# Performance work log

Hardware: AMD Instinct MI355X
Metric: run time of the kernel (lower is better)

The kernel has to match this reference:

```python
import jax, jax.numpy as jnp
import numpy as np

HEAD_NUMS = 8
LN_EPS = 1e-5


def _layernorm(x, g, b):
    m = jnp.mean(x, axis=-1, keepdims=True)
    v = jnp.var(x, axis=-1, keepdims=True)
    return (x - m) * jax.lax.rsqrt(v + LN_EPS) * g + b


def setup_inputs() -> dict:
    key = jax.random.key(0)
    ks = jax.random.split(key, 6)
    B, S, D = 4, 2048, 512
    x = jax.random.normal(ks[0], (B, S, D), dtype=jnp.float32)
    W1 = jax.random.normal(ks[1], (4 * D, D), dtype=jnp.float32) * 0.02
    b1 = jnp.zeros((4 * D,), dtype=jnp.float32)
    ln_g = jnp.ones((D,), dtype=jnp.float32)
    ln_b = jnp.zeros((D,), dtype=jnp.float32)
    W2 = jax.random.normal(ks[2], (D, D), dtype=jnp.float32) * 0.02
    b2 = jnp.zeros((D,), dtype=jnp.float32)
    return {"x": x, "W1": W1, "b1": b1, "ln_g": ln_g, "ln_b": ln_b, "W2": W2, "b2": b2}


def reference(x, W1, b1, ln_g, ln_b, W2, b2):
    B, S, D = x.shape
    H = HEAD_NUMS
    hd = D // H
    # fused qkv+gate projection with SiLU (HSTU style)
    h = jax.nn.silu(x @ W1.T + b1)                   # [B,S,4D]
    h = h.reshape(B, S, 4, H, hd)                    # split into gate,q,k,v
    gate = jnp.transpose(h[:, :, 0], (0, 2, 1, 3))   # [B,H,S,hd]
    q = jnp.transpose(h[:, :, 1], (0, 2, 1, 3))
    k = jnp.transpose(h[:, :, 2], (0, 2, 1, 3))
    v = jnp.transpose(h[:, :, 3], (0, 2, 1, 3))
    scale = 1.0 / np.sqrt(hd).astype(np.float32)
    scores = jnp.einsum('bhsd,bhtd->bhst', q, k) * scale   # [B,H,S,S]
    causal = jnp.tril(jnp.ones((S, S), dtype=bool))        # allowed: t <= s
    # silu replaces softmax; masked (future) positions contribute 0
    # (mathematical limit of silu(-inf) is 0)
    a = jnp.where(causal, jax.nn.silu(scores), 0.0)
    o = jnp.einsum('bhst,bhtd->bhsd', a, v)                # [B,H,S,hd]
    o = jnp.transpose(o, (0, 2, 1, 3)).reshape(B, S, D)
    normed = _layernorm(o, ln_g, ln_b)
    gate_f = jnp.transpose(gate, (0, 2, 1, 3)).reshape(B, S, D)
    return (normed * gate_f) @ W2.T + b2
```

## Files before the change

### kernel.cpp

```cpp
#include <hip/hip_runtime.h>
#include <cstdint>


typedef __attribute__((ext_vector_type(8))) short short8;
typedef __attribute__((ext_vector_type(4))) float f32x4;

__device__ __forceinline__ unsigned short f2bf(float f) {
  union { float f; unsigned u; } v; v.f = f;
  unsigned r = v.u + 0x7FFFu + ((v.u >> 16) & 1u);
  return (unsigned short)(r >> 16);
}
__device__ __forceinline__ float bf2f(unsigned short h) {
  union { unsigned u; float f; } v; v.u = ((unsigned)h) << 16; return v.f;
}
__device__ __forceinline__ float silu_f(float x) {
  return x / (1.0f + __expf(-x));
}
__device__ __forceinline__ void gl_lds16(const void* g, void* l) {
  __builtin_amdgcn_global_load_lds(
      (const __attribute__((address_space(1))) void*)g,
      (__attribute__((address_space(3))) void*)l, 16, 0, 0);
}

__global__ void convert_kernel(const float* __restrict__ x, const float* __restrict__ w1,
                               const float* __restrict__ w2,
                               unsigned short* __restrict__ xb, unsigned short* __restrict__ w1b,
                               unsigned short* __restrict__ w2b) {
  int i = blockIdx.x * 256 + threadIdx.x;
  const float* s; unsigned short* d;
  if (i < 1048576) { s = x; d = xb; }
  else if (i < 1048576 + 262144) { i -= 1048576; s = w1; d = w1b; }
  else { i -= (1048576 + 262144); if (i >= 65536) return; s = w2; d = w2b; }
  float4 f = ((const float4*)s)[i];
  ushort4 o; o.x = f2bf(f.x); o.y = f2bf(f.y); o.z = f2bf(f.z); o.w = f2bf(f.w);
  ((ushort4*)d)[i] = o;
}

__global__ __launch_bounds__(256, 2) void gemm1_kernel(
    const unsigned short* __restrict__ xb,
    const unsigned short* __restrict__ w1b,
    const float* __restrict__ b1,
    unsigned short* __restrict__ h,
    unsigned short* __restrict__ vt)
{
  __shared__ __align__(16) unsigned short As[16 * 528];
  __shared__ __align__(16) unsigned short Bs[16 * 528];
  const int tid = threadIdx.x;
  const int w = tid >> 6, l = tid & 63;
  const int bm = blockIdx.x & 63, bn = blockIdx.x >> 6;
  const int wm = w & 1, wn = w >> 1;
  const int quad = l >> 4, lc = l & 15;
  const int r8 = l >> 3, c8 = l & 7;
  const int lanebase = (lc >> 3) * 528 + (lc & 7) * 64 + quad * 8;

  f32x4 acc[4][4] = {};

  const unsigned short* ga = xb + (size_t)(bm * 128 + w * 32 + r8) * 512 + c8 * 8;
  const unsigned short* gb = w1b + (size_t)(bn * 128 + w * 32 + r8) * 512 + c8 * 8;

  for (int kt = 0; kt < 512; kt += 64) {
#pragma unroll
    for (int i = 0; i < 4; ++i) {
      gl_lds16(ga + i * 8 * 512 + kt, As + (w * 4 + i) * 528);
      gl_lds16(gb + i * 8 * 512 + kt, Bs + (w * 4 + i) * 528);
    }
    __syncthreads();
#pragma unroll
    for (int kk = 0; kk < 2; ++kk) {
      short8 af[4], bf[4];
#pragma unroll
      for (int mt = 0; mt < 4; ++mt)
        af[mt] = *(const short8*)(As + (wm * 8 + mt * 2) * 528 + lanebase + kk * 32);
#pragma unroll
      for (int nt = 0; nt < 4; ++nt)
        bf[nt] = *(const short8*)(Bs + (wn * 8 + nt * 2) * 528 + lanebase + kk * 32);
#pragma unroll
      for (int mt = 0; mt < 4; ++mt)
#pragma unroll
        for (int nt = 0; nt < 4; ++nt)
          acc[mt][nt] = __builtin_amdgcn_mfma_f32_16x16x32_bf16(af[mt], bf[nt], acc[mt][nt], 0, 0, 0);
    }
    __syncthreads();
  }

  const int sec = bn >> 2;
  if (sec == 3) {
#pragma unroll
    for (int nt = 0; nt < 4; ++nt) {
      const int n = bn * 128 + wn * 64 + nt * 16 + lc;
      const float bias = b1[n];
      const int hh = (n >> 6) & 7, d = n & 63;
#pragma unroll
      for (int mt = 0; mt < 4; ++mt) {
        const int m0 = bm * 128 + wm * 64 + mt * 16 + quad * 4;
        const int b = m0 >> 11, s = m0 & 2047;
        ushort4 pk;
        pk.x = f2bf(silu_f(acc[mt][nt][0] + bias));
        pk.y = f2bf(silu_f(acc[mt][nt][1] + bias));
        pk.z = f2bf(silu_f(acc[mt][nt][2] + bias));
        pk.w = f2bf(silu_f(acc[mt][nt][3] + bias));
        *(ushort4*)(vt + (size_t)((b * 8 + hh) * 64 + d) * 2048 + s) = pk;
      }
    }
  } else {
    const float osc = (sec == 1) ? 0.125f : 1.0f;
#pragma unroll
    for (int nt = 0; nt < 4; ++nt) {
      const int n = bn * 128 + wn * 64 + nt * 16 + lc;
      const float bias = b1[n];
#pragma unroll
      for (int mt = 0; mt < 4; ++mt) {
        const int m0 = bm * 128 + wm * 64 + mt * 16 + quad * 4;
#pragma unroll
        for (int r = 0; r < 4; ++r)
          h[(size_t)(m0 + r) * 2048 + n] = f2bf(silu_f(acc[mt][nt][r] + bias) * osc);
      }
    }
  }
}

__global__ __launch_bounds__(256, 3) void attn_kernel(
    const unsigned short* __restrict__ h,
    const unsigned short* __restrict__ vt,
    float* __restrict__ o)
{
  __shared__ __align__(16) unsigned short Ks[16 * 528];
  __shared__ __align__(16) unsigned short Vs[16 * 528];
  __shared__ __align__(16) unsigned short Ps[64 * 136];
  const int tid = threadIdx.x;
  const int w = tid >> 6, l = tid & 63;
  const int bh = blockIdx.x & 31;
  const int qi = 31 - (blockIdx.x >> 5);
  const int b = bh >> 3, hh = bh & 7;
  const int quad = l >> 4, lc = l & 15;
  const int r8 = l >> 3, c8 = l & 7;
  const int wm = w & 1, wn = w >> 1;
  const int q0 = qi * 64;
  const int nk = (qi >> 1) + 1;
  const int klanebase = (lc >> 3) * 528 + (lc & 7) * 64 + quad * 8;

  {
    const unsigned short* qg =
        h + (size_t)(b * 2048 + q0 + w * 16 + r8) * 2048 + 512 + hh * 64 + c8 * 8;
#pragma unroll
    for (int i = 0; i < 2; ++i)
      gl_lds16(qg + (size_t)i * 8 * 2048, Ks + (w * 16 + i * 8) * 64);
  }
  __syncthreads();
  short8 qf[2][2];
#pragma unroll
  for (int nt = 0; nt < 2; ++nt)
#pragma unroll
    for (int kk = 0; kk < 2; ++kk)
      qf[nt][kk] = *(const short8*)(Ks + (wn * 32 + nt * 16 + lc) * 64 + kk * 32 + quad * 8);

  f32x4 oacc[4] = {};

  const unsigned short* kg =
      h + (size_t)(b * 2048 + w * 32 + r8) * 2048 + 1024 + hh * 64 + c8 * 8;
  const unsigned short* vg = vt + (size_t)(bh * 64 + w * 16 + quad) * 2048 + lc * 8;

  for (int ti = 0; ti < nk; ++ti) {
    __syncthreads();
    const int toff = ti * 128;
#pragma unroll
    for (int i = 0; i < 4; ++i) {
      gl_lds16(kg + (size_t)(toff + i * 8) * 2048, Ks + (w * 4 + i) * 528);
      gl_lds16(vg + (size_t)(i * 4) * 2048 + toff, Vs + (w * 4 + i) * 528);
    }
    __syncthreads();

    f32x4 sc[4][2] = {};
#pragma unroll
    for (int kk = 0; kk < 2; ++kk) {
      short8 kf[4];
#pragma unroll
      for (int mt = 0; mt < 4; ++mt)
        kf[mt] = *(const short8*)(Ks + (wm * 8 + mt * 2) * 528 + klanebase + kk * 32);
#pragma unroll
      for (int mt = 0; mt < 4; ++mt)
#pragma unroll
        for (int nt = 0; nt < 2; ++nt)
          sc[mt][nt] = __builtin_amdgcn_mfma_f32_16x16x32_bf16(kf[mt], qf[nt][kk], sc[mt][nt], 0, 0, 0);
    }

    if (ti < nk - 1) {
#pragma unroll
      for (int mt = 0; mt < 4; ++mt) {
        const int tloc = wm * 64 + mt * 16 + quad * 4;
#pragma unroll
        for (int nt = 0; nt < 2; ++nt) {
          const int qloc = wn * 32 + nt * 16 + lc;
          ushort4 pk;
          pk.x = f2bf(silu_f(sc[mt][nt][0]));
          pk.y = f2bf(silu_f(sc[mt][nt][1]));
          pk.z = f2bf(silu_f(sc[mt][nt][2]));
          pk.w = f2bf(silu_f(sc[mt][nt][3]));
          *(ushort4*)(Ps + qloc * 136 + tloc) = pk;
        }
      }
    } else {
#pragma unroll
      for (int mt = 0; mt < 4; ++mt) {
        const int tloc = wm * 64 + mt * 16 + quad * 4;
        const int tg = toff + tloc;
#pragma unroll
        for (int nt = 0; nt < 2; ++nt) {
          const int qloc = wn * 32 + nt * 16 + lc;
          const int qg = q0 + qloc;
          ushort4 pk;
          pk.x = (tg + 0 <= qg) ? f2bf(silu_f(sc[mt][nt][0])) : (unsigned short)0;
          pk.y = (tg + 1 <= qg) ? f2bf(silu_f(sc[mt][nt][1])) : (unsigned short)0;
          pk.z = (tg + 2 <= qg) ? f2bf(silu_f(sc[mt][nt][2])) : (unsigned short)0;
          pk.w = (tg + 3 <= qg) ? f2bf(silu_f(sc[mt][nt][3])) : (unsigned short)0;
          *(ushort4*)(Ps + qloc * 136 + tloc) = pk;
        }
      }
    }
    __syncthreads();

#pragma unroll
    for (int ks = 0; ks < 4; ++ks) {
      short8 pf = *(const short8*)(Ps + (w * 16 + lc) * 136 + ks * 32 + quad * 8);
#pragma unroll
      for (int nt = 0; nt < 4; ++nt) {
        short8 vf = *(const short8*)(Vs + (nt * 4 + (lc >> 2)) * 528 + (lc & 3) * 128 +
                                     ks * 32 + quad * 8);
        oacc[nt] = __builtin_amdgcn_mfma_f32_16x16x32_bf16(pf, vf, oacc[nt], 0, 0, 0);
      }
    }
  }

  float* og = o + (size_t)(b * 2048 + q0 + w * 16) * 512 + hh * 64;
#pragma unroll
  for (int nt = 0; nt < 4; ++nt)
#pragma unroll
    for (int r = 0; r < 4; ++r)
      og[(quad * 4 + r) * 512 + nt * 16 + lc] = oacc[nt][r];
}

__global__ __launch_bounds__(256) void ln_gate_kernel(
    const float* __restrict__ o, const unsigned short* __restrict__ h,
    const float* __restrict__ lng, const float* __restrict__ lnb,
    unsigned short* __restrict__ y) {
  const int row = blockIdx.x * 4 + (threadIdx.x >> 6);
  const int l = threadIdx.x & 63;
  const float4* orow = (const float4*)(o + (size_t)row * 512);
  float4 a = orow[l * 2], c = orow[l * 2 + 1];
  float s0 = a.x + a.y + a.z + a.w + c.x + c.y + c.z + c.w;
#pragma unroll
  for (int off = 32; off > 0; off >>= 1) s0 += __shfl_xor(s0, off);
  const float mean = s0 * (1.0f / 512.0f);
  float dx[8] = {a.x - mean, a.y - mean, a.z - mean, a.w - mean,
                 c.x - mean, c.y - mean, c.z - mean, c.w - mean};
  float sq = 0.f;
#pragma unroll
  for (int j = 0; j < 8; ++j) sq += dx[j] * dx[j];
#pragma unroll
  for (int off = 32; off > 0; off >>= 1) sq += __shfl_xor(sq, off);
  const float inv = rsqrtf(sq * (1.0f / 512.0f) + 1e-5f);
  const float4* g4 = (const float4*)lng;
  const float4* b4 = (const float4*)lnb;
  float4 g0 = g4[l * 2], g1 = g4[l * 2 + 1], bb0 = b4[l * 2], bb1 = b4[l * 2 + 1];
  const unsigned short* grow = h + (size_t)row * 2048;
  ushort4 gr0 = *(const ushort4*)(grow + l * 8);
  ushort4 gr1 = *(const ushort4*)(grow + l * 8 + 4);
  float gg[8] = {g0.x, g0.y, g0.z, g0.w, g1.x, g1.y, g1.z, g1.w};
  float bbv[8] = {bb0.x, bb0.y, bb0.z, bb0.w, bb1.x, bb1.y, bb1.z, bb1.w};
  float gv[8] = {bf2f(gr0.x), bf2f(gr0.y), bf2f(gr0.z), bf2f(gr0.w),
                 bf2f(gr1.x), bf2f(gr1.y), bf2f(gr1.z), bf2f(gr1.w)};
  ushort4 p0, p1;
  p0.x = f2bf((dx[0] * inv * gg[0] + bbv[0]) * gv[0]);
  p0.y = f2bf((dx[1] * inv * gg[1] + bbv[1]) * gv[1]);
  p0.z = f2bf((dx[2] * inv * gg[2] + bbv[2]) * gv[2]);
  p0.w = f2bf((dx[3] * inv * gg[3] + bbv[3]) * gv[3]);
  p1.x = f2bf((dx[4] * inv * gg[4] + bbv[4]) * gv[4]);
  p1.y = f2bf((dx[5] * inv * gg[5] + bbv[5]) * gv[5]);
  p1.z = f2bf((dx[6] * inv * gg[6] + bbv[6]) * gv[6]);
  p1.w = f2bf((dx[7] * inv * gg[7] + bbv[7]) * gv[7]);
  ushort4* yrow = (ushort4*)(y + (size_t)row * 512);
  yrow[l * 2] = p0;
  yrow[l * 2 + 1] = p1;
}

__global__ __launch_bounds__(256, 2) void gemm2_kernel(
    const unsigned short* __restrict__ yb,
    const unsigned short* __restrict__ w2b,
    const float* __restrict__ b2, float* __restrict__ out) {
  __shared__ __align__(16) unsigned short As[16 * 528];
  __shared__ __align__(16) unsigned short Bs[16 * 528];
  const int tid = threadIdx.x;
  const int w = tid >> 6, l = tid & 63;
  const int bm = blockIdx.x & 63, bn = blockIdx.x >> 6;
  const int wm = w & 1, wn = w >> 1;
  const int quad = l >> 4, lc = l & 15;
  const int r8 = l >> 3, c8 = l & 7;
  const int lanebase = (lc >> 3) * 528 + (lc & 7) * 64 + quad * 8;

  f32x4 acc[4][4] = {};
  const unsigned short* ga = yb + (size_t)(bm * 128 + w * 32 + r8) * 512 + c8 * 8;
  const unsigned short* gb = w2b + (size_t)(bn * 128 + w * 32 + r8) * 512 + c8 * 8;

  for (int kt = 0; kt < 512; kt += 64) {
#pragma unroll
    for (int i = 0; i < 4; ++i) {
      gl_lds16(ga + i * 8 * 512 + kt, As + (w * 4 + i) * 528);
      gl_lds16(gb + i * 8 * 512 + kt, Bs + (w * 4 + i) * 528);
    }
    __syncthreads();
#pragma unroll
    for (int kk = 0; kk < 2; ++kk) {
      short8 af[4], bf[4];
#pragma unroll
      for (int mt = 0; mt < 4; ++mt)
        af[mt] = *(const short8*)(As + (wm * 8 + mt * 2) * 528 + lanebase + kk * 32);
#pragma unroll
      for (int nt = 0; nt < 4; ++nt)
        bf[nt] = *(const short8*)(Bs + (wn * 8 + nt * 2) * 528 + lanebase + kk * 32);
#pragma unroll
      for (int mt = 0; mt < 4; ++mt)
#pragma unroll
        for (int nt = 0; nt < 4; ++nt)
          acc[mt][nt] = __builtin_amdgcn_mfma_f32_16x16x32_bf16(af[mt], bf[nt], acc[mt][nt], 0, 0, 0);
    }
    __syncthreads();
  }

#pragma unroll
  for (int nt = 0; nt < 4; ++nt) {
    const int n = bn * 128 + wn * 64 + nt * 16 + lc;
    const float bias = b2[n];
#pragma unroll
    for (int mt = 0; mt < 4; ++mt) {
      const int m0 = bm * 128 + wm * 64 + mt * 16 + quad * 4;
#pragma unroll
      for (int r = 0; r < 4; ++r)
        out[(size_t)(m0 + r) * 512 + n] = acc[mt][nt][r] + bias;
    }
  }
}

extern "C" void kernel_launch(void* const* d_in, const int* in_sizes, int n_in,
                              void* d_out, int out_size, void* d_ws, size_t ws_size,
                              hipStream_t stream) {
  const float* x = (const float*)d_in[0];
  const float* W1 = (const float*)d_in[1];
  const float* b1 = (const float*)d_in[2];
  const float* lng = (const float*)d_in[3];
  const float* lnb = (const float*)d_in[4];
  const float* W2 = (const float*)d_in[5];
  const float* b2 = (const float*)d_in[6];
  float* out = (float*)d_out;
  char* ws = (char*)d_ws;

  unsigned short* xb  = (unsigned short*)(ws);
  unsigned short* w1b = (unsigned short*)(ws + 8388608);
  unsigned short* w2b = (unsigned short*)(ws + 10485760);
  unsigned short* h   = (unsigned short*)(ws + 11010048);
  unsigned short* vt  = (unsigned short*)(ws + 44564480);
  float* o            = (float*)(ws + 52953088);
  unsigned short* yb  = (unsigned short*)(ws + 69730304);

  convert_kernel<<<5376, 256, 0, stream>>>(x, W1, W2, xb, w1b, w2b);
  gemm1_kernel<<<1024, 256, 0, stream>>>(xb, w1b, b1, h, vt);
  attn_kernel<<<1024, 256, 0, stream>>>(h, vt, o);
  ln_gate_kernel<<<2048, 256, 0, stream>>>(o, h, lng, lnb, yb);
  gemm2_kernel<<<256, 256, 0, stream>>>(yb, w2b, b2, out);
}
```

Before: 182.5 us.

## XOR-swizzle LDS tiles, stage GEMM1 epilogue through LDS, faster SiLU and bf16 packing

```diff
diff --git a/kernel.cpp b/kernel.cpp
--- a/kernel.cpp
+++ b/kernel.cpp
@@ -1,4 +1,5 @@
 #include <hip/hip_runtime.h>
+#include <hip/hip_bf16.h>
 #include <cstdint>
 
 
@@ -13,8 +14,27 @@
 __device__ __forceinline__ float bf2f(unsigned short h) {
   union { unsigned u; float f; } v; v.u = ((unsigned)h) << 16; return v.f;
 }
+__device__ __forceinline__ float fast_rcp(float x) {
+#if __has_builtin(__builtin_amdgcn_rcpf)
+  return __builtin_amdgcn_rcpf(x);
+#else
+  return 1.0f / x;
+#endif
+}
+__device__ __forceinline__ float fast_exp2(float x) {
+#if __has_builtin(__builtin_amdgcn_exp2f)
+  return __builtin_amdgcn_exp2f(x);
+#else
+  return exp2f(x);
+#endif
+}
 __device__ __forceinline__ float silu_f(float x) {
-  return x / (1.0f + __expf(-x));
+  return x * fast_rcp(1.0f + fast_exp2(-1.442695041f * x));
+}
+__device__ __forceinline__ unsigned pk2(float lo, float hi) {
+  union { __hip_bfloat162 b; unsigned u; } cv;
+  cv.b = __float22bfloat162_rn(make_float2(lo, hi));
+  return cv.u;
 }
 __device__ __forceinline__ void gl_lds16(const void* g, void* l) {
   __builtin_amdgcn_global_load_lds(
@@ -32,8 +52,8 @@
   else if (i < 1048576 + 262144) { i -= 1048576; s = w1; d = w1b; }
   else { i -= (1048576 + 262144); if (i >= 65536) return; s = w2; d = w2b; }
   float4 f = ((const float4*)s)[i];
-  ushort4 o; o.x = f2bf(f.x); o.y = f2bf(f.y); o.z = f2bf(f.z); o.w = f2bf(f.w);
-  ((ushort4*)d)[i] = o;
+  uint2 o; o.x = pk2(f.x, f.y); o.y = pk2(f.z, f.w);
+  ((uint2*)d)[i] = o;
 }
 
 __global__ __launch_bounds__(256, 2) void gemm1_kernel(
@@ -43,26 +63,25 @@
     unsigned short* __restrict__ h,
     unsigned short* __restrict__ vt)
 {
-  __shared__ __align__(16) unsigned short As[16 * 528];
-  __shared__ __align__(16) unsigned short Bs[16 * 528];
+  __shared__ __align__(16) unsigned short smem[16896];
+  unsigned short* As = smem;
+  unsigned short* Bs = smem + 8192;
   const int tid = threadIdx.x;
   const int w = tid >> 6, l = tid & 63;
   const int bm = blockIdx.x & 63, bn = blockIdx.x >> 6;
   const int wm = w & 1, wn = w >> 1;
-  const int quad = l >> 4, lc = l & 15;
-  const int r8 = l >> 3, c8 = l & 7;
-  const int lanebase = (lc >> 3) * 528 + (lc & 7) * 64 + quad * 8;
+  const int quad = l >> 4, lc = l & 15, lc7 = lc & 7;
+  const int r8 = l >> 3, c8 = (l & 7) ^ r8;
 
   f32x4 acc[4][4] = {};
-
   const unsigned short* ga = xb + (size_t)(bm * 128 + w * 32 + r8) * 512 + c8 * 8;
   const unsigned short* gb = w1b + (size_t)(bn * 128 + w * 32 + r8) * 512 + c8 * 8;
 
   for (int kt = 0; kt < 512; kt += 64) {
 #pragma unroll
     for (int i = 0; i < 4; ++i) {
-      gl_lds16(ga + i * 8 * 512 + kt, As + (w * 4 + i) * 528);
-      gl_lds16(gb + i * 8 * 512 + kt, Bs + (w * 4 + i) * 528);
+      gl_lds16(ga + i * 8 * 512 + kt, As + (w * 4 + i) * 512);
+      gl_lds16(gb + i * 8 * 512 + kt, Bs + (w * 4 + i) * 512);
     }
     __syncthreads();
 #pragma unroll
@@ -70,10 +89,12 @@
       short8 af[4], bf[4];
 #pragma unroll
       for (int mt = 0; mt < 4; ++mt)
-        af[mt] = *(const short8*)(As + (wm * 8 + mt * 2) * 528 + lanebase + kk * 32);
+        af[mt] = *(const short8*)(As + (wm * 64 + mt * 16 + lc) * 64 +
+                                  (((kk * 4 + quad) ^ lc7) * 8));
 #pragma unroll
       for (int nt = 0; nt < 4; ++nt)
-        bf[nt] = *(const short8*)(Bs + (wn * 8 + nt * 2) * 528 + lanebase + kk * 32);
+        bf[nt] = *(const short8*)(Bs + (wn * 64 + nt * 16 + lc) * 64 +
+                                  (((kk * 4 + quad) ^ lc7) * 8));
 #pragma unroll
       for (int mt = 0; mt < 4; ++mt)
 #pragma unroll
@@ -83,38 +104,54 @@
     __syncthreads();
   }
 
+  unsigned short* T = smem;
   const int sec = bn >> 2;
   if (sec == 3) {
 #pragma unroll
     for (int nt = 0; nt < 4; ++nt) {
-      const int n = bn * 128 + wn * 64 + nt * 16 + lc;
-      const float bias = b1[n];
-      const int hh = (n >> 6) & 7, d = n & 63;
+      const int nl = wn * 64 + nt * 16 + lc;
+      const float bias = b1[bn * 128 + nl];
 #pragma unroll
       for (int mt = 0; mt < 4; ++mt) {
-        const int m0 = bm * 128 + wm * 64 + mt * 16 + quad * 4;
-        const int b = m0 >> 11, s = m0 & 2047;
-        ushort4 pk;
-        pk.x = f2bf(silu_f(acc[mt][nt][0] + bias));
-        pk.y = f2bf(silu_f(acc[mt][nt][1] + bias));
-        pk.z = f2bf(silu_f(acc[mt][nt][2] + bias));
-        pk.w = f2bf(silu_f(acc[mt][nt][3] + bias));
-        *(ushort4*)(vt + (size_t)((b * 8 + hh) * 64 + d) * 2048 + s) = pk;
+        const int sl = wm * 64 + mt * 16 + quad * 4;
+        uint2 pk;
+        pk.x = pk2(silu_f(acc[mt][nt][0] + bias), silu_f(acc[mt][nt][1] + bias));
+        pk.y = pk2(silu_f(acc[mt][nt][2] + bias), silu_f(acc[mt][nt][3] + bias));
+        *(uint2*)(T + nl * 132 + sl) = pk;
       }
     }
   } else {
     const float osc = (sec == 1) ? 0.125f : 1.0f;
 #pragma unroll
     for (int nt = 0; nt < 4; ++nt) {
-      const int n = bn * 128 + wn * 64 + nt * 16 + lc;
-      const float bias = b1[n];
+      const int nl = wn * 64 + nt * 16 + lc;
+      const float bias = b1[bn * 128 + nl];
 #pragma unroll
       for (int mt = 0; mt < 4; ++mt) {
-        const int m0 = bm * 128 + wm * 64 + mt * 16 + quad * 4;
+        const int sl = wm * 64 + mt * 16 + quad * 4;
 #pragma unroll
         for (int r = 0; r < 4; ++r)
-          h[(size_t)(m0 + r) * 2048 + n] = f2bf(silu_f(acc[mt][nt][r] + bias) * osc);
+          T[(sl + r) * 132 + nl] = f2bf(silu_f(acc[mt][nt][r] + bias) * osc);
       }
+    }
+  }
+  __syncthreads();
+  const int rrow = tid >> 4, rcol = (tid & 15) * 8;
+  if (sec == 3) {
+    const int bq = bm >> 4, sbase = (bm & 15) * 128;
+#pragma unroll
+    for (int p = 0; p < 8; ++p) {
+      const int row = p * 16 + rrow;
+      const int n = bn * 128 + row, hh = (n >> 6) & 7, d = n & 63;
+      *(short8*)(vt + (size_t)((bq * 8 + hh) * 64 + d) * 2048 + sbase + rcol) =
+          *(const short8*)(T + row * 132 + rcol);
+    }
+  } else {
+#pragma unroll
+    for (int p = 0; p < 8; ++p) {
+      const int row = p * 16 + rrow;
+      *(short8*)(h + (size_t)(bm * 128 + row) * 2048 + bn * 128 + rcol) =
+          *(const short8*)(T + row * 132 + rcol);
     }
   }
 }
@@ -124,27 +161,26 @@
     const unsigned short* __restrict__ vt,
     float* __restrict__ o)
 {
-  __shared__ __align__(16) unsigned short Ks[16 * 528];
-  __shared__ __align__(16) unsigned short Vs[16 * 528];
+  __shared__ __align__(16) unsigned short Ks[128 * 64];
+  __shared__ __align__(16) unsigned short Vs[64 * 128];
   __shared__ __align__(16) unsigned short Ps[64 * 136];
   const int tid = threadIdx.x;
   const int w = tid >> 6, l = tid & 63;
   const int bh = blockIdx.x & 31;
   const int qi = 31 - (blockIdx.x >> 5);
   const int b = bh >> 3, hh = bh & 7;
-  const int quad = l >> 4, lc = l & 15;
-  const int r8 = l >> 3, c8 = l & 7;
+  const int quad = l >> 4, lc = l & 15, lc7 = lc & 7;
+  const int r8 = l >> 3, c8 = (l & 7) ^ r8;
   const int wm = w & 1, wn = w >> 1;
   const int q0 = qi * 64;
   const int nk = (qi >> 1) + 1;
-  const int klanebase = (lc >> 3) * 528 + (lc & 7) * 64 + quad * 8;
 
   {
     const unsigned short* qg =
         h + (size_t)(b * 2048 + q0 + w * 16 + r8) * 2048 + 512 + hh * 64 + c8 * 8;
 #pragma unroll
     for (int i = 0; i < 2; ++i)
-      gl_lds16(qg + (size_t)i * 8 * 2048, Ks + (w * 16 + i * 8) * 64);
+      gl_lds16(qg + (size_t)i * 8 * 2048, Ks + (w * 2 + i) * 512);
   }
   __syncthreads();
   short8 qf[2][2];
@@ -152,21 +188,27 @@
   for (int nt = 0; nt < 2; ++nt)
 #pragma unroll
     for (int kk = 0; kk < 2; ++kk)
-      qf[nt][kk] = *(const short8*)(Ks + (wn * 32 + nt * 16 + lc) * 64 + kk * 32 + quad * 8);
+      qf[nt][kk] = *(const short8*)(Ks + (wn * 32 + nt * 16 + lc) * 64 +
+                                    (((kk * 4 + quad) ^ lc7) * 8));
 
   f32x4 oacc[4] = {};
 
   const unsigned short* kg =
       h + (size_t)(b * 2048 + w * 32 + r8) * 2048 + 1024 + hh * 64 + c8 * 8;
-  const unsigned short* vg = vt + (size_t)(bh * 64 + w * 16 + quad) * 2048 + lc * 8;
+  const int vrow = l >> 4, vcol = l & 15;
+  const unsigned short* vgE =
+      vt + (size_t)(bh * 64 + w * 16 + vrow) * 2048 + ((vcol ^ vrow) * 8);
+  const unsigned short* vgO =
+      vt + (size_t)(bh * 64 + w * 16 + vrow) * 2048 + ((vcol ^ vrow ^ 4) * 8);
 
   for (int ti = 0; ti < nk; ++ti) {
     __syncthreads();
     const int toff = ti * 128;
 #pragma unroll
     for (int i = 0; i < 4; ++i) {
-      gl_lds16(kg + (size_t)(toff + i * 8) * 2048, Ks + (w * 4 + i) * 528);
-      gl_lds16(vg + (size_t)(i * 4) * 2048 + toff, Vs + (w * 4 + i) * 528);
+      gl_lds16(kg + (size_t)(toff + i * 8) * 2048, Ks + (w * 4 + i) * 512);
+      const unsigned short* vsrc = ((i & 1) ? vgO : vgE) + (size_t)(i * 4) * 2048 + toff;
+      gl_lds16(vsrc, Vs + (w * 4 + i) * 512);
     }
     __syncthreads();
 
@@ -176,7 +218,8 @@
       short8 kf[4];
 #pragma unroll
       for (int mt = 0; mt < 4; ++mt)
-        kf[mt] = *(const short8*)(Ks + (wm * 8 + mt * 2) * 528 + klanebase + kk * 32);
+        kf[mt] = *(const short8*)(Ks + (wm * 64 + mt * 16 + lc) * 64 +
+                                  (((kk * 4 + quad) ^ lc7) * 8));
 #pragma unroll
       for (int mt = 0; mt < 4; ++mt)
 #pragma unroll
@@ -191,12 +234,10 @@
 #pragma unroll
         for (int nt = 0; nt < 2; ++nt) {
           const int qloc = wn * 32 + nt * 16 + lc;
-          ushort4 pk;
-          pk.x = f2bf(silu_f(sc[mt][nt][0]));
-          pk.y = f2bf(silu_f(sc[mt][nt][1]));
-          pk.z = f2bf(silu_f(sc[mt][nt][2]));
-          pk.w = f2bf(silu_f(sc[mt][nt][3]));
-          *(ushort4*)(Ps + qloc * 136 + tloc) = pk;
+          uint2 pk;
+          pk.x = pk2(silu_f(sc[mt][nt][0]), silu_f(sc[mt][nt][1]));
+          pk.y = pk2(silu_f(sc[mt][nt][2]), silu_f(sc[mt][nt][3]));
+          *(uint2*)(Ps + qloc * 136 + tloc) = pk;
         }
       }
     } else {
@@ -208,12 +249,12 @@
         for (int nt = 0; nt < 2; ++nt) {
           const int qloc = wn * 32 + nt * 16 + lc;
           const int qg = q0 + qloc;
-          ushort4 pk;
-          pk.x = (tg + 0 <= qg) ? f2bf(silu_f(sc[mt][nt][0])) : (unsigned short)0;
-          pk.y = (tg + 1 <= qg) ? f2bf(silu_f(sc[mt][nt][1])) : (unsigned short)0;
-          pk.z = (tg + 2 <= qg) ? f2bf(silu_f(sc[mt][nt][2])) : (unsigned short)0;
-          pk.w = (tg + 3 <= qg) ? f2bf(silu_f(sc[mt][nt][3])) : (unsigned short)0;
-          *(ushort4*)(Ps + qloc * 136 + tloc) = pk;
+          float v0 = (tg + 0 <= qg) ? silu_f(sc[mt][nt][0]) : 0.0f;
+          float v1 = (tg + 1 <= qg) ? silu_f(sc[mt][nt][1]) : 0.0f;
+          float v2 = (tg + 2 <= qg) ? silu_f(sc[mt][nt][2]) : 0.0f;
+          float v3 = (tg + 3 <= qg) ? silu_f(sc[mt][nt][3]) : 0.0f;
+          uint2 pk; pk.x = pk2(v0, v1); pk.y = pk2(v2, v3);
+          *(uint2*)(Ps + qloc * 136 + tloc) = pk;
         }
       }
     }
@@ -224,8 +265,8 @@
       short8 pf = *(const short8*)(Ps + (w * 16 + lc) * 136 + ks * 32 + quad * 8);
 #pragma unroll
       for (int nt = 0; nt < 4; ++nt) {
-        short8 vf = *(const short8*)(Vs + (nt * 4 + (lc >> 2)) * 528 + (lc & 3) * 128 +
-                                     ks * 32 + quad * 8);
+        short8 vf = *(const short8*)(Vs + (nt * 16 + lc) * 128 +
+                                     (((ks * 4 + quad) ^ lc7) * 8));
         oacc[nt] = __builtin_amdgcn_mfma_f32_16x16x32_bf16(pf, vf, oacc[nt], 0, 0, 0);
       }
     }
@@ -269,16 +310,13 @@
   float bbv[8] = {bb0.x, bb0.y, bb0.z, bb0.w, bb1.x, bb1.y, bb1.z, bb1.w};
   float gv[8] = {bf2f(gr0.x), bf2f(gr0.y), bf2f(gr0.z), bf2f(gr0.w),
                  bf2f(gr1.x), bf2f(gr1.y), bf2f(gr1.z), bf2f(gr1.w)};
-  ushort4 p0, p1;
-  p0.x = f2bf((dx[0] * inv * gg[0] + bbv[0]) * gv[0]);
-  p0.y = f2bf((dx[1] * inv * gg[1] + bbv[1]) * gv[1]);
-  p0.z = f2bf((dx[2] * inv * gg[2] + bbv[2]) * gv[2]);
-  p0.w = f2bf((dx[3] * inv * gg[3] + bbv[3]) * gv[3]);
-  p1.x = f2bf((dx[4] * inv * gg[4] + bbv[4]) * gv[4]);
-  p1.y = f2bf((dx[5] * inv * gg[5] + bbv[5]) * gv[5]);
-  p1.z = f2bf((dx[6] * inv * gg[6] + bbv[6]) * gv[6]);
-  p1.w = f2bf((dx[7] * inv * gg[7] + bbv[7]) * gv[7]);
-  ushort4* yrow = (ushort4*)(y + (size_t)row * 512);
+  float r[8];
+#pragma unroll
+  for (int j = 0; j < 8; ++j) r[j] = (dx[j] * inv * gg[j] + bbv[j]) * gv[j];
+  uint2 p0, p1;
+  p0.x = pk2(r[0], r[1]); p0.y = pk2(r[2], r[3]);
+  p1.x = pk2(r[4], r[5]); p1.y = pk2(r[6], r[7]);
+  uint2* yrow = (uint2*)(y + (size_t)row * 512);
   yrow[l * 2] = p0;
   yrow[l * 2 + 1] = p1;
 }
@@ -287,15 +325,14 @@
     const unsigned short* __restrict__ yb,
     const unsigned short* __restrict__ w2b,
     const float* __restrict__ b2, float* __restrict__ out) {
-  __shared__ __align__(16) unsigned short As[16 * 528];
-  __shared__ __align__(16) unsigned short Bs[16 * 528];
+  __shared__ __align__(16) unsigned short As[128 * 64];
+  __shared__ __align__(16) unsigned short Bs[128 * 64];
   const int tid = threadIdx.x;
   const int w = tid >> 6, l = tid & 63;
   const int bm = blockIdx.x & 63, bn = blockIdx.x >> 6;
   const int wm = w & 1, wn = w >> 1;
-  const int quad = l >> 4, lc = l & 15;
-  const int r8 = l >> 3, c8 = l & 7;
-  const int lanebase = (lc >> 3) * 528 + (lc & 7) * 64 + quad * 8;
+  const int quad = l >> 4, lc = l & 15, lc7 = lc & 7;
+  const int r8 = l >> 3, c8 = (l & 7) ^ r8;
 
   f32x4 acc[4][4] = {};
   const unsigned short* ga = yb + (size_t)(bm * 128 + w * 32 + r8) * 512 + c8 * 8;
@@ -304,8 +341,8 @@
   for (int kt = 0; kt < 512; kt += 64) {
 #pragma unroll
     for (int i = 0; i < 4; ++i) {
-      gl_lds16(ga + i * 8 * 512 + kt, As + (w * 4 + i) * 528);
-      gl_lds16(gb + i * 8 * 512 + kt, Bs + (w * 4 + i) * 528);
+      gl_lds16(ga + i * 8 * 512 + kt, As + (w * 4 + i) * 512);
+      gl_lds16(gb + i * 8 * 512 + kt, Bs + (w * 4 + i) * 512);
     }
     __syncthreads();
 #pragma unroll
@@ -313,10 +350,12 @@
       short8 af[4], bf[4];
 #pragma unroll
       for (int mt = 0; mt < 4; ++mt)
-        af[mt] = *(const short8*)(As + (wm * 8 + mt * 2) * 528 + lanebase + kk * 32);
+        af[mt] = *(const short8*)(As + (wm * 64 + mt * 16 + lc) * 64 +
+                                  (((kk * 4 + quad) ^ lc7) * 8));
 #pragma unroll
       for (int nt = 0; nt < 4; ++nt)
-        bf[nt] = *(const short8*)(Bs + (wn * 8 + nt * 2) * 528 + lanebase + kk * 32);
+        bf[nt] = *(const short8*)(Bs + (wn * 64 + nt * 16 + lc) * 64 +
+                                  (((kk * 4 + quad) ^ lc7) * 8));
 #pragma unroll
       for (int mt = 0; mt < 4; ++mt)
 #pragma unroll
```

After: 158.9 us. 1.15x faster.
